# Kernel optimization log

Measured on AMD Instinct MI355X. Metric: run time of the kernel, lower is better.

The kernel has to match this reference:

```python
import jax, jax.numpy as jnp
import numpy as np

B, N, D_OBS, D_NB = 8192, 64, 128, 128
HEADS, GAT_F, GRU_H = 4, 64, 256
ACTION_DIM = 16
PERIOD0 = 24.0
NEG_SLOPE = 0.2
PMAX, PBUDGET = 0.5, 1.0
ENC_DIM = D_OBS + 1  # feature 0 expands to sin/cos
FUSE_IN = ENC_DIM + HEADS * GAT_F


def cyclical_encode(x):
    phase = 2.0 * jnp.pi * x[:, 0] / PERIOD0
    return jnp.concatenate([jnp.sin(phase)[:, None], jnp.cos(phase)[:, None], x[:, 1:]], axis=1)


def gat(node_feat, neigh_feat, mask, W, a):
    # node_feat [B,Din], neigh_feat [B,N,Din], W [Din,H*F], a [H,2F,1]
    b, n, _ = neigh_feat.shape
    h_node = (node_feat @ W).reshape(b, HEADS, GAT_F)            # [B,H,F]
    h_nb = (neigh_feat @ W).reshape(b, n, HEADS, GAT_F)          # [B,N,H,F]
    a_src, a_dst = a[:, :GAT_F, 0], a[:, GAT_F:, 0]              # [H,F] each
    e = (jnp.einsum('bhf,hf->bh', h_node, a_src)[:, None, :]
         + jnp.einsum('bnhf,hf->bnh', h_nb, a_dst))              # [B,N,H]
    e = jnp.where(e > 0, e, NEG_SLOPE * e)                        # leaky_relu
    e = jnp.where(mask[:, :, None], e, -jnp.inf)
    alpha = jax.nn.softmax(e, axis=1)                             # over neighbors
    agg = jnp.einsum('bnh,bnhf->bhf', alpha, h_nb)
    return agg.reshape(b, HEADS * GAT_F)


def gru_cell(x, h, Wih, bih, Whh, bhh):
    gi = x @ Wih + bih
    gh = h @ Whh + bhh
    ir, iz, in_ = jnp.split(gi, 3, axis=-1)
    hr, hz, hn = jnp.split(gh, 3, axis=-1)
    r = jax.nn.sigmoid(ir + hr)
    z = jax.nn.sigmoid(iz + hz)
    nn_ = jnp.tanh(in_ + r * hn)
    return (1.0 - z) * nn_ + z * h


def layer_norm(x, g, b, eps=1e-5):
    mu = jnp.mean(x, axis=-1, keepdims=True)
    var = jnp.var(x, axis=-1, keepdims=True)
    return (x - mu) * jax.lax.rsqrt(var + eps) * g + b


def project_power(raw):
    # Euclidean projection onto {0<=p<=PMAX, sum p<=PBUDGET} via bisection on mu
    def total(mu):
        return jnp.sum(jnp.clip(raw - mu[:, None], 0.0, PMAX), axis=1)
    feas = total(jnp.zeros(raw.shape[0], raw.dtype)) <= PBUDGET
    lo = jnp.zeros(raw.shape[0], raw.dtype)
    hi = jnp.maximum(jnp.max(raw, axis=1), 0.0)
    def body(_, lh):
        lo, hi = lh
        mid = 0.5 * (lo + hi)
        over = total(mid) > PBUDGET
        return (jnp.where(over, mid, lo), jnp.where(over, hi, mid))
    lo, hi = jax.lax.fori_loop(0, 60, body, (lo, hi))
    mu = jnp.where(feas, 0.0, hi)
    return jnp.clip(raw - mu[:, None], 0.0, PMAX)


def setup_inputs() -> dict:
    key = jax.random.key(0)
    ks = jax.random.split(key, 20)
    def init(k, shape, fan_in):
        return (jax.random.normal(k, shape, jnp.float32) / np.sqrt(fan_in)).astype(jnp.float32)
    mask = jax.random.bernoulli(ks[3], 0.5, (B, N))
    mask = mask.at[:, 0].set(True)  # guarantee >=1 valid neighbor per row
    return {
        'node_obs': jax.random.normal(ks[0], (B, D_OBS), jnp.float32),
        'neighbor_obs': jax.random.normal(ks[1], (B, N, D_NB), jnp.float32),
        'neighbor_mask': mask,
        'hidden_state': jnp.zeros((1, B, GRU_H), jnp.float32),
        'W_gat': init(ks[4], (D_NB, HEADS * GAT_F), D_NB),
        'a_gat': init(ks[5], (HEADS, 2 * GAT_F, 1), 2 * GAT_F),
        'fusion_W': init(ks[6], (FUSE_IN, GRU_H), FUSE_IN),
        'fusion_b': jnp.zeros((GRU_H,), jnp.float32),
        'Wih': init(ks[7], (GRU_H, 3 * GRU_H), GRU_H),
        'bih': jnp.zeros((3 * GRU_H,), jnp.float32),
        'Whh': init(ks[8], (GRU_H, 3 * GRU_H), GRU_H),
        'bhh': jnp.zeros((3 * GRU_H,), jnp.float32),
        'ln_g': jnp.ones((GRU_H,), jnp.float32),
        'ln_b': jnp.zeros((GRU_H,), jnp.float32),
        'W1': init(ks[9], (GRU_H, 256), GRU_H),
        'b1': jnp.zeros((256,), jnp.float32),
        'W2': init(ks[10], (256, 128), 256),
        'b2': jnp.zeros((128,), jnp.float32),
        'W3': init(ks[11], (128, ACTION_DIM), 128),
        'b3': jnp.zeros((ACTION_DIM,), jnp.float32),
    }


def reference(node_obs, neighbor_obs, neighbor_mask, hidden_state,
              W_gat, a_gat, fusion_W, fusion_b, Wih, bih, Whh, bhh,
              ln_g, ln_b, W1, b1, W2, b2, W3, b3):
    enc = cyclical_encode(node_obs)                              # [B, ENC_DIM]
    node_feat_for_gat = neighbor_obs[:, 0, :]
    ctx = gat(node_feat_for_gat, neighbor_obs, neighbor_mask, W_gat, a_gat)
    fused = jax.nn.relu(jnp.concatenate([enc, ctx], axis=-1) @ fusion_W + fusion_b)
    h_new = gru_cell(fused, hidden_state[0], Wih, bih, Whh, bhh)  # 1-step GRU
    belief = layer_norm(h_new, ln_g, ln_b)
    x = jax.nn.relu(belief @ W1 + b1)
    x = jax.nn.relu(x @ W2 + b2)
    raw = x @ W3 + b3                                            # [B, ACTION_DIM]
    action = project_power(raw)
    return action, h_new[None, :, :]
```

## Files before the change

### kernel.cpp

```cpp
#include <hip/hip_runtime.h>
#include <hip/hip_bf16.h>


typedef unsigned short u16;
typedef unsigned int   u32;
typedef __attribute__((ext_vector_type(8))) short bf16x8;
typedef __attribute__((ext_vector_type(4))) float f32x4;

#define KFUSE  672
#define ACT_TOT (8192*16)

__device__ __forceinline__ u16 f2bf(float x){
  u32 u = __float_as_uint(x);
  u += 0x7fffu + ((u >> 16) & 1u);
  return (u16)(u >> 16);
}
__device__ __forceinline__ float bf2f(u16 h){ return __uint_as_float(((u32)h) << 16); }

__device__ __forceinline__ void frag_one(const float* __restrict__ src, int ld, int col0,
                                         int NT, u16* __restrict__ dhi, u16* __restrict__ dlo,
                                         int f, int fsrc, int l){
  int kt = fsrc / NT, nt = fsrc % NT;
  int kbase = kt*32 + (l >> 4)*8, n = col0 + nt*16 + (l & 15);
  size_t o = ((size_t)f*64 + l)*8;
  #pragma unroll
  for(int i = 0; i < 8; ++i){
    float w = src[(size_t)(kbase + i)*ld + n];
    u16 h = f2bf(w);
    dhi[o + i] = h;
    dlo[o + i] = f2bf(w - bf2f(h));
  }
}

__device__ __forceinline__ void frag_wbig(const float* __restrict__ fW,
                                          const float* __restrict__ Wg,
                                          u16* __restrict__ dhi, u16* __restrict__ dlo,
                                          int f, int l){
  int kt = f / 16, nt = f % 16;
  int kbase = kt*32 + (l >> 4)*8, n = nt*16 + (l & 15);
  size_t o = ((size_t)f*64 + l)*8;
  #pragma unroll
  for(int i = 0; i < 8; ++i){
    int r = kbase + i;
    float v;
    if(r < 129) v = fW[(size_t)r*256 + n];
    else if(r < 641){
      int h = (r - 129) >> 7, kk = (r - 129) & 127;
      float s = 0.f;
      for(int ff = 0; ff < 64; ++ff)
        s += Wg[kk*256 + h*64 + ff] * fW[(size_t)(129 + h*64 + ff)*256 + n];
      v = s;
    } else v = 0.f;
    u16 hh = f2bf(v);
    dhi[o + i] = hh;
    dlo[o + i] = f2bf(v - bf2f(hh));
  }
}

#define P_FF0   1
#define P_WRZ0  85
#define P_WIN0  213
#define P_WHN0  245
#define P_F10   277
#define P_F20   309
#define P_SP0   325
__global__ __launch_bounds__(256) void k_prep(
    const unsigned char* __restrict__ maskb, int* __restrict__ flag,
    const float* __restrict__ Wg, const float* __restrict__ ag,
    float* __restrict__ was, float* __restrict__ wad,
    const float* __restrict__ fW,
    const float* __restrict__ Wih, const float* __restrict__ Whh,
    const float* __restrict__ W1, const float* __restrict__ W2,
    u16* __restrict__ ffh, u16* __restrict__ ffl,
    u16* __restrict__ wrzh, u16* __restrict__ wrzl,
    u16* __restrict__ winh, u16* __restrict__ winl,
    u16* __restrict__ whnh, u16* __restrict__ whnl,
    u16* __restrict__ f1h, u16* __restrict__ f1l,
    u16* __restrict__ f2h, u16* __restrict__ f2l,
    const float* __restrict__ hidden, u16* __restrict__ acath, u16* __restrict__ acatl)
{
  int bx = blockIdx.x, t = threadIdx.x;
  if(bx == 0){
    if(t == 0){
      int s = 0;
      for(int i = 1; i < 256; i += 4) s += maskb[i];
      *flag = (s == 0) ? 1 : 0;
    }
    #pragma unroll
    for(int v = 0; v < 2; ++v){
      int idx = v*256 + t, k = idx & 127, h = idx >> 7;
      float s = 0.f, d = 0.f;
      for(int f = 0; f < 64; ++f){
        float w = Wg[k*256 + h*64 + f];
        s += w * ag[h*128 + f];
        d += w * ag[h*128 + 64 + f];
      }
      was[k*4 + h] = s; wad[k*4 + h] = d;
    }
  } else if(bx < P_WRZ0){
    int sub = t >> 6, l = t & 63;
    int f = (bx - P_FF0)*4 + sub;
    frag_wbig(fW, Wg, ffh, ffl, f, l);
  } else if(bx < P_SP0){
    int sub = t >> 6, l = t & 63;
    if(bx < P_WIN0){
      int idx = (bx - P_WRZ0)*4 + sub;
      if(idx < 256) frag_one(Wih, 768, 0, 32, wrzh, wrzl, idx, idx, l);
      else          frag_one(Whh, 768, 0, 32, wrzh, wrzl, idx, idx - 256, l);
    } else if(bx < P_WHN0){
      int f = (bx - P_WIN0)*4 + sub;
      frag_one(Wih, 768, 512, 16, winh, winl, f, f, l);
    } else if(bx < P_F10){
      int f = (bx - P_WHN0)*4 + sub;
      frag_one(Whh, 768, 512, 16, whnh, whnl, f, f, l);
    } else if(bx < P_F20){
      int f = (bx - P_F10)*4 + sub;
      frag_one(W1, 256, 0, 16, f1h, f1l, f, f, l);
    } else {
      int f = (bx - P_F20)*4 + sub;
      frag_one(W2, 128, 0, 8, f2h, f2l, f, f, l);
    }
  } else {
    int i = (bx - P_SP0)*256 + t;
    int idx8 = i*8, row = idx8 >> 8, col = idx8 & 255;
    const float4* p = (const float4*)(hidden + (size_t)idx8);
    float4 v0 = p[0], v1 = p[1];
    float vv[8] = {v0.x,v0.y,v0.z,v0.w,v1.x,v1.y,v1.z,v1.w};
    u16 h8[8], l8[8];
    #pragma unroll
    for(int q = 0; q < 8; ++q){ u16 h = f2bf(vv[q]); h8[q] = h; l8[q] = f2bf(vv[q] - bf2f(h)); }
    uint4 uh = { (u32)h8[0] | ((u32)h8[1]<<16), (u32)h8[2] | ((u32)h8[3]<<16),
                 (u32)h8[4] | ((u32)h8[5]<<16), (u32)h8[6] | ((u32)h8[7]<<16) };
    uint4 ul = { (u32)l8[0] | ((u32)l8[1]<<16), (u32)l8[2] | ((u32)l8[3]<<16),
                 (u32)l8[4] | ((u32)l8[5]<<16), (u32)l8[6] | ((u32)l8[7]<<16) };
    size_t off = (size_t)row*512 + 256 + col;
    *(uint4*)(acath + off) = uh;
    *(uint4*)(acatl + off) = ul;
  }
}

__global__ __launch_bounds__(256) void k_gat(
    const float* __restrict__ nbg, const float* __restrict__ node,
    const void* __restrict__ maskp, const int* __restrict__ flagp,
    const float* __restrict__ was, const float* __restrict__ wad,
    u16* __restrict__ xhi, u16* __restrict__ xlo)
{
  __shared__ float s_nb[8192];
  __shared__ float s_wad[512];
  __shared__ float s_ep[1024];
  __shared__ float s_alpha[256];
  int b = blockIdx.x, t = threadIdx.x;
  const float* nb = nbg + (size_t)b*8192;
  const int isint = *flagp;

  s_wad[t] = wad[t]; s_wad[t+256] = wad[t+256];

  #pragma unroll
  for(int q = 0; q < 8; ++q){
    int f = q*256 + t;
    int n = f >> 5, ch = f & 31;
    float4 v = *(const float4*)(nb + f*4);
    *(float4*)(s_nb + (n*32 + (ch ^ (n & 31)))*4) = v;
  }

  if(t < 129){
    float v;
    if(t < 2){
      float ph = node[(size_t)b*128] * (6.2831853071795864769f / 24.0f);
      v = (t == 0) ? sinf(ph) : cosf(ph);
    } else v = node[(size_t)b*128 + (t-1)];
    u16 h = f2bf(v);
    size_t o = (size_t)b*KFUSE + t;
    xhi[o] = h; xlo[o] = f2bf(v - bf2f(h));
  } else if(t < 160){
    size_t o = (size_t)b*KFUSE + 641 + (t - 129);
    xhi[o] = 0; xlo[o] = 0;
  }
  __syncthreads();

  {
    int n = t & 63, c = t >> 6;
    float adx = 0.f, ady = 0.f, adz = 0.f, adw = 0.f;
    #pragma unroll
    for(int q = 0; q < 8; ++q){
      int ch = c*8 + q;
      float4 v = *(const float4*)(s_nb + (n*32 + (ch ^ (n & 31)))*4);
      float vv[4] = {v.x, v.y, v.z, v.w};
      #pragma unroll
      for(int i2 = 0; i2 < 4; ++i2){
        int k = ch*4 + i2;
        float4 wd = *(const float4*)(s_wad + k*4);
        adx += vv[i2]*wd.x; ady += vv[i2]*wd.y; adz += vv[i2]*wd.z; adw += vv[i2]*wd.w;
      }
    }
    float4 ad = {adx, ady, adz, adw};
    *(float4*)(s_ep + (c*64 + n)*4) = ad;
  }
  __syncthreads();

  {
    int n2 = t & 63, h2 = t >> 6;
    float es = 0.f;
    #pragma unroll
    for(int ii = 0; ii < 2; ++ii){
      int k = n2*2 + ii;
      float v0 = s_nb[(k >> 2)*4 + (k & 3)];
      es += v0 * was[k*4 + h2];
    }
    for(int off = 32; off; off >>= 1) es += __shfl_xor(es, off);
    float ed = s_ep[n2*4 + h2] + s_ep[(64+n2)*4 + h2]
             + s_ep[(128+n2)*4 + h2] + s_ep[(192+n2)*4 + h2];
    float e = es + ed;
    e = (e > 0.f) ? e : 0.2f*e;
    bool valid;
    if(isint) valid = ((const u32*)maskp)[(size_t)b*64 + n2] != 0u;
    else      valid = ((const unsigned char*)maskp)[(size_t)b*64 + n2] != 0;
    float ev = valid ? e : -1e30f;
    float m = ev;
    for(int off = 32; off; off >>= 1) m = fmaxf(m, __shfl_xor(m, off));
    float p = valid ? expf(ev - m) : 0.f;
    float s = p;
    for(int off = 32; off; off >>= 1) s += __shfl_xor(s, off);
    s_alpha[n2*4 + h2] = p / s;
  }
  __syncthreads();

  {
    int c2 = t & 31, hp = (t >> 6) & 1, half = t >> 7;
    int sub = (t >> 5) & 1;
    float4 a0 = {0.f,0.f,0.f,0.f}, a1 = {0.f,0.f,0.f,0.f};
    int nbase = half*32 + sub*16;
    #pragma unroll
    for(int i = 0; i < 16; ++i){
      int n = nbase + i;
      float4 v = *(const float4*)(s_nb + (n*32 + (c2 ^ (n & 31)))*4);
      float2 ap = *(const float2*)(s_alpha + n*4 + hp*2);
      a0.x += ap.x*v.x; a0.y += ap.x*v.y; a0.z += ap.x*v.z; a0.w += ap.x*v.w;
      a1.x += ap.y*v.x; a1.y += ap.y*v.y; a1.z += ap.y*v.z; a1.w += ap.y*v.w;
    }
    a0.x += __shfl_xor(a0.x, 32); a0.y += __shfl_xor(a0.y, 32);
    a0.z += __shfl_xor(a0.z, 32); a0.w += __shfl_xor(a0.w, 32);
    a1.x += __shfl_xor(a1.x, 32); a1.y += __shfl_xor(a1.y, 32);
    a1.z += __shfl_xor(a1.z, 32); a1.w += __shfl_xor(a1.w, 32);
    __syncthreads();
    if((t & 63) < 32){
      int w = t >> 6;
      *(float4*)(s_ep + (w*32 + c2)*8 + 0) = a0;
      *(float4*)(s_ep + (w*32 + c2)*8 + 4) = a1;
    }
  }
  __syncthreads();
  if(t < 128){
    int h = t >> 5, cc = t & 31;
    int hp2 = h >> 1, slot = h & 1;
    float4 p0 = *(const float4*)(s_ep + ((0*2 + hp2)*32 + cc)*8 + slot*4);
    float4 p1 = *(const float4*)(s_ep + ((1*2 + hp2)*32 + cc)*8 + slot*4);
    float vv[4] = {p0.x+p1.x, p0.y+p1.y, p0.z+p1.z, p0.w+p1.w};
    size_t o = (size_t)b*KFUSE + 129 + h*128 + cc*4;
    #pragma unroll
    for(int i = 0; i < 4; ++i){
      u16 hh = f2bf(vv[i]);
      xhi[o+i] = hh; xlo[o+i] = f2bf(vv[i] - bf2f(hh));
    }
  }
}

template<int KT, int NT_TOT, int NPW, int ROWF>
__global__ __launch_bounds__(256) void k_gemm3(
    const u16* __restrict__ xhi, const u16* __restrict__ xlo, int lda,
    const u16* __restrict__ wfhi, const u16* __restrict__ wflo,
    const float* __restrict__ bias,
    u16* __restrict__ ohi, u16* __restrict__ olo, int ost, int ocol)
{
  int l = threadIdx.x & 63, w = threadIdx.x >> 6;
  int m0 = blockIdx.x * (16*ROWF);
  int ntbase = blockIdx.y * (4*NPW) + w*NPW;
  f32x4 acc[NPW][ROWF];
  #pragma unroll
  for(int j = 0; j < NPW; ++j)
    #pragma unroll
    for(int rf = 0; rf < ROWF; ++rf) acc[j][rf] = (f32x4){0.f,0.f,0.f,0.f};
  size_t arow[ROWF];
  #pragma unroll
  for(int rf = 0; rf < ROWF; ++rf)
    arow[rf] = (size_t)(m0 + rf*16 + (l & 15))*lda + (size_t)((l >> 4)*8);
  bf16x8 ah[ROWF], al[ROWF];
  #pragma unroll
  for(int rf = 0; rf < ROWF; ++rf){
    ah[rf] = *(const bf16x8*)(xhi + arow[rf]);
    al[rf] = *(const bf16x8*)(xlo + arow[rf]);
  }
  for(int kt = 0; kt < KT; ++kt){
    bf16x8 ahn[ROWF], aln[ROWF];
    if(kt + 1 < KT){
      #pragma unroll
      for(int rf = 0; rf < ROWF; ++rf){
        ahn[rf] = *(const bf16x8*)(xhi + arow[rf] + (kt+1)*32);
        aln[rf] = *(const bf16x8*)(xlo + arow[rf] + (kt+1)*32);
      }
    }
    #pragma unroll
    for(int j = 0; j < NPW; ++j){
      size_t bo = ((size_t)(kt*NT_TOT + ntbase + j)*64 + l)*8;
      bf16x8 bh = *(const bf16x8*)(wfhi + bo);
      bf16x8 bl = *(const bf16x8*)(wflo + bo);
      #pragma unroll
      for(int rf = 0; rf < ROWF; ++rf){
        acc[j][rf] = __builtin_amdgcn_mfma_f32_16x16x32_bf16(ah[rf], bh, acc[j][rf], 0, 0, 0);
        acc[j][rf] = __builtin_amdgcn_mfma_f32_16x16x32_bf16(ah[rf], bl, acc[j][rf], 0, 0, 0);
        acc[j][rf] = __builtin_amdgcn_mfma_f32_16x16x32_bf16(al[rf], bh, acc[j][rf], 0, 0, 0);
      }
    }
    #pragma unroll
    for(int rf = 0; rf < ROWF; ++rf){ ah[rf] = ahn[rf]; al[rf] = aln[rf]; }
  }
  #pragma unroll
  for(int j = 0; j < NPW; ++j){
    int col = (ntbase + j)*16 + (l & 15);
    float bv = bias[col];
    #pragma unroll
    for(int rf = 0; rf < ROWF; ++rf){
      int r0 = m0 + rf*16 + (l >> 4)*4;
      #pragma unroll
      for(int q = 0; q < 4; ++q){
        float y = fmaxf(acc[j][rf][q] + bv, 0.f);
        size_t o = (size_t)(r0 + q)*ost + ocol + col;
        u16 h = f2bf(y);
        ohi[o] = h; olo[o] = f2bf(y - bf2f(h));
      }
    }
  }
}

#define BSTR 264
#define XSTR 132
__global__ __launch_bounds__(512) void k_grumlp(
    const u16* __restrict__ ah_, const u16* __restrict__ al_,
    const u16* __restrict__ wrzh, const u16* __restrict__ wrzl,
    const u16* __restrict__ winh, const u16* __restrict__ winl,
    const u16* __restrict__ whnh, const u16* __restrict__ whnl,
    const u16* __restrict__ f1h, const u16* __restrict__ f1l,
    const u16* __restrict__ f2h, const u16* __restrict__ f2l,
    const float* __restrict__ bih, const float* __restrict__ bhh,
    const float* __restrict__ hidden, const float* __restrict__ lng,
    const float* __restrict__ lnb,
    const float* __restrict__ b1, const float* __restrict__ b2,
    const float* __restrict__ W3, const float* __restrict__ b3,
    float* __restrict__ hout, float* __restrict__ act)
{
  __shared__ float s_s1[256], s_s2[256], s_mu[32], s_rs[32];
  __shared__ u16 s_bh[32*BSTR], s_bl[32*BSTR];
  __shared__ float s_x2[32*XSTR];
  __shared__ float sW3[2048];
  int t = threadIdx.x;
  int l = t & 63, w = t >> 6;
  int m0 = blockIdx.x*32;
  for(int i = t; i < 2048; i += 512) sW3[i] = W3[i];

  f32x4 ar[2][2], az[2][2], aa[2][2], ab[2][2];
  #pragma unroll
  for(int j = 0; j < 2; ++j)
    #pragma unroll
    for(int rf = 0; rf < 2; ++rf){
      ar[j][rf] = (f32x4){0.f,0.f,0.f,0.f}; az[j][rf] = (f32x4){0.f,0.f,0.f,0.f};
      aa[j][rf] = (f32x4){0.f,0.f,0.f,0.f}; ab[j][rf] = (f32x4){0.f,0.f,0.f,0.f};
    }
  size_t arow[2];
  #pragma unroll
  for(int rf = 0; rf < 2; ++rf)
    arow[rf] = (size_t)(m0 + rf*16 + (l & 15))*512 + (size_t)((l >> 4)*8);
  for(int kt = 0; kt < 16; ++kt){
    bf16x8 xh[2], xl[2];
    #pragma unroll
    for(int rf = 0; rf < 2; ++rf){
      xh[rf] = *(const bf16x8*)(ah_ + arow[rf] + kt*32);
      xl[rf] = *(const bf16x8*)(al_ + arow[rf] + kt*32);
    }
    #pragma unroll
    for(int j = 0; j < 2; ++j){
      int nt = w*2 + j;
      size_t bo = ((size_t)(kt*32 + nt)*64 + l)*8;
      bf16x8 bh = *(const bf16x8*)(wrzh + bo);
      bf16x8 bl = *(const bf16x8*)(wrzl + bo);
      size_t bo2 = bo + (size_t)16*64*8;
      bf16x8 bh2 = *(const bf16x8*)(wrzh + bo2);
      bf16x8 bl2 = *(const bf16x8*)(wrzl + bo2);
      #pragma unroll
      for(int rf = 0; rf < 2; ++rf){
        ar[j][rf] = __builtin_amdgcn_mfma_f32_16x16x32_bf16(xh[rf], bh, ar[j][rf], 0, 0, 0);
        ar[j][rf] = __builtin_amdgcn_mfma_f32_16x16x32_bf16(xh[rf], bl, ar[j][rf], 0, 0, 0);
        ar[j][rf] = __builtin_amdgcn_mfma_f32_16x16x32_bf16(xl[rf], bh, ar[j][rf], 0, 0, 0);
        az[j][rf] = __builtin_amdgcn_mfma_f32_16x16x32_bf16(xh[rf], bh2, az[j][rf], 0, 0, 0);
        az[j][rf] = __builtin_amdgcn_mfma_f32_16x16x32_bf16(xh[rf], bl2, az[j][rf], 0, 0, 0);
        az[j][rf] = __builtin_amdgcn_mfma_f32_16x16x32_bf16(xl[rf], bh2, az[j][rf], 0, 0, 0);
      }
    }
  }
  for(int kt = 0; kt < 8; ++kt){
    bf16x8 fh[2], fl2[2], gh[2], gl[2];
    #pragma unroll
    for(int rf = 0; rf < 2; ++rf){
      fh[rf]  = *(const bf16x8*)(ah_ + arow[rf] + kt*32);
      fl2[rf] = *(const bf16x8*)(al_ + arow[rf] + kt*32);
      gh[rf]  = *(const bf16x8*)(ah_ + arow[rf] + 256 + kt*32);
      gl[rf]  = *(const bf16x8*)(al_ + arow[rf] + 256 + kt*32);
    }
    #pragma unroll
    for(int j = 0; j < 2; ++j){
      int nt = w*2 + j;
      size_t bo = ((size_t)(kt*16 + nt)*64 + l)*8;
      bf16x8 bh = *(const bf16x8*)(winh + bo);
      bf16x8 bl = *(const bf16x8*)(winl + bo);
      bf16x8 ch = *(const bf16x8*)(whnh + bo);
      bf16x8 cl2 = *(const bf16x8*)(whnl + bo);
      #pragma unroll
      for(int rf = 0; rf < 2; ++rf){
        aa[j][rf] = __builtin_amdgcn_mfma_f32_16x16x32_bf16(fh[rf], bh, aa[j][rf], 0, 0, 0);
        aa[j][rf] = __builtin_amdgcn_mfma_f32_16x16x32_bf16(fh[rf], bl, aa[j][rf], 0, 0, 0);
        aa[j][rf] = __builtin_amdgcn_mfma_f32_16x16x32_bf16(fl2[rf], bh, aa[j][rf], 0, 0, 0);
        ab[j][rf] = __builtin_amdgcn_mfma_f32_16x16x32_bf16(gh[rf], ch, ab[j][rf], 0, 0, 0);
        ab[j][rf] = __builtin_amdgcn_mfma_f32_16x16x32_bf16(gh[rf], cl2, ab[j][rf], 0, 0, 0);
        ab[j][rf] = __builtin_amdgcn_mfma_f32_16x16x32_bf16(gl[rf], ch, ab[j][rf], 0, 0, 0);
      }
    }
  }
  int cl = l & 15, rq = l >> 4;
  float hnew[2][2][4];
  float s1p[2][4], s2p[2][4];
  #pragma unroll
  for(int rf = 0; rf < 2; ++rf)
    #pragma unroll
    for(int q = 0; q < 4; ++q){ s1p[rf][q] = 0.f; s2p[rf][q] = 0.f; }
  #pragma unroll
  for(int j = 0; j < 2; ++j){
    int col = w*32 + j*16 + cl;
    float br = bih[col] + bhh[col];
    float bz = bih[256+col] + bhh[256+col];
    float bi = bih[512+col];
    float bh2 = bhh[512+col];
    #pragma unroll
    for(int rf = 0; rf < 2; ++rf){
      #pragma unroll
      for(int q = 0; q < 4; ++q){
        int row = m0 + rf*16 + rq*4 + q;
        float rs = ar[j][rf][q] + br;
        float zs = az[j][rf][q] + bz;
        float in_ = aa[j][rf][q] + bi;
        float hn  = ab[j][rf][q] + bh2;
        float h   = hidden[(size_t)row*256 + col];
        float r = 1.f/(1.f + expf(-rs));
        float z = 1.f/(1.f + expf(-zs));
        float nv = tanhf(in_ + r*hn);
        float hv = (1.f - z)*nv + z*h;
        hnew[j][rf][q] = hv;
        hout[(size_t)row*256 + col] = hv;
        s1p[rf][q] += hv; s2p[rf][q] += hv*hv;
      }
    }
  }
  #pragma unroll
  for(int rf = 0; rf < 2; ++rf)
    #pragma unroll
    for(int q = 0; q < 4; ++q){
      float a = s1p[rf][q], b2v = s2p[rf][q];
      for(int off = 1; off < 16; off <<= 1){
        a += __shfl_xor(a, off); b2v += __shfl_xor(b2v, off);
      }
      if(cl == 0){
        int rloc = rf*16 + rq*4 + q;
        s_s1[w*32 + rloc] = a; s_s2[w*32 + rloc] = b2v;
      }
    }
  __syncthreads();
  if(t < 32){
    int rloc = t;
    float t1 = 0.f, t2 = 0.f;
    #pragma unroll
    for(int ww = 0; ww < 8; ++ww){ t1 += s_s1[ww*32 + rloc]; t2 += s_s2[ww*32 + rloc]; }
    float mu = t1 * (1.f/256.f);
    float var = t2 * (1.f/256.f) - mu*mu;
    s_mu[rloc] = mu; s_rs[rloc] = rsqrtf(var + 1e-5f);
  }
  __syncthreads();
  #pragma unroll
  for(int j = 0; j < 2; ++j){
    int col = w*32 + j*16 + cl;
    float g = lng[col], bb = lnb[col];
    #pragma unroll
    for(int rf = 0; rf < 2; ++rf){
      #pragma unroll
      for(int q = 0; q < 4; ++q){
        int rloc = rf*16 + rq*4 + q;
        float bel = (hnew[j][rf][q] - s_mu[rloc]) * s_rs[rloc] * g + bb;
        u16 hb = f2bf(bel);
        s_bh[rloc*BSTR + col] = hb;
        s_bl[rloc*BSTR + col] = f2bf(bel - bf2f(hb));
      }
    }
  }
  __syncthreads();
  f32x4 ax1[2][2];
  #pragma unroll
  for(int j = 0; j < 2; ++j)
    #pragma unroll
    for(int rf = 0; rf < 2; ++rf) ax1[j][rf] = (f32x4){0.f,0.f,0.f,0.f};
  for(int kt = 0; kt < 8; ++kt){
    bf16x8 xh[2], xl[2];
    #pragma unroll
    for(int rf = 0; rf < 2; ++rf){
      int off = (rf*16 + (l & 15))*BSTR + kt*32 + (l >> 4)*8;
      xh[rf] = *(const bf16x8*)(s_bh + off);
      xl[rf] = *(const bf16x8*)(s_bl + off);
    }
    #pragma unroll
    for(int j = 0; j < 2; ++j){
      size_t bo = ((size_t)(kt*16 + w*2 + j)*64 + l)*8;
      bf16x8 bh = *(const bf16x8*)(f1h + bo);
      bf16x8 bl = *(const bf16x8*)(f1l + bo);
      #pragma unroll
      for(int rf = 0; rf < 2; ++rf){
        ax1[j][rf] = __builtin_amdgcn_mfma_f32_16x16x32_bf16(xh[rf], bh, ax1[j][rf], 0, 0, 0);
        ax1[j][rf] = __builtin_amdgcn_mfma_f32_16x16x32_bf16(xh[rf], bl, ax1[j][rf], 0, 0, 0);
        ax1[j][rf] = __builtin_amdgcn_mfma_f32_16x16x32_bf16(xl[rf], bh, ax1[j][rf], 0, 0, 0);
      }
    }
  }
  __syncthreads();
  #pragma unroll
  for(int j = 0; j < 2; ++j){
    int col = (w*2 + j)*16 + cl;
    float bv = b1[col];
    #pragma unroll
    for(int rf = 0; rf < 2; ++rf){
      #pragma unroll
      for(int q = 0; q < 4; ++q){
        int rloc = rf*16 + rq*4 + q;
        float y = fmaxf(ax1[j][rf][q] + bv, 0.f);
        u16 hh = f2bf(y);
        s_bh[rloc*BSTR + col] = hh;
        s_bl[rloc*BSTR + col] = f2bf(y - bf2f(hh));
      }
    }
  }
  __syncthreads();
  f32x4 ax2[2];
  #pragma unroll
  for(int rf = 0; rf < 2; ++rf) ax2[rf] = (f32x4){0.f,0.f,0.f,0.f};
  for(int kt = 0; kt < 8; ++kt){
    bf16x8 xh[2], xl[2];
    #pragma unroll
    for(int rf = 0; rf < 2; ++rf){
      int off = (rf*16 + (l & 15))*BSTR + kt*32 + (l >> 4)*8;
      xh[rf] = *(const bf16x8*)(s_bh + off);
      xl[rf] = *(const bf16x8*)(s_bl + off);
    }
    size_t bo = ((size_t)(kt*8 + w)*64 + l)*8;
    bf16x8 bh = *(const bf16x8*)(f2h + bo);
    bf16x8 bl = *(const bf16x8*)(f2l + bo);
    #pragma unroll
    for(int rf = 0; rf < 2; ++rf){
      ax2[rf] = __builtin_amdgcn_mfma_f32_16x16x32_bf16(xh[rf], bh, ax2[rf], 0, 0, 0);
      ax2[rf] = __builtin_amdgcn_mfma_f32_16x16x32_bf16(xh[rf], bl, ax2[rf], 0, 0, 0);
      ax2[rf] = __builtin_amdgcn_mfma_f32_16x16x32_bf16(xl[rf], bh, ax2[rf], 0, 0, 0);
    }
  }
  {
    int col = w*16 + cl;
    float bv = b2[col];
    #pragma unroll
    for(int rf = 0; rf < 2; ++rf)
      #pragma unroll
      for(int q = 0; q < 4; ++q){
        int rloc = rf*16 + rq*4 + q;
        s_x2[rloc*XSTR + col] = fmaxf(ax2[rf][q] + bv, 0.f);
      }
  }
  __syncthreads();
  {
    int j = t & 15, rl = t >> 4;
    const float* xr = s_x2 + rl*XSTR;
    float raw = b3[j];
    #pragma unroll 8
    for(int k4 = 0; k4 < 32; ++k4){
      float4 v = *(const float4*)(xr + k4*4);
      raw += v.x*sW3[(k4*4+0)*16 + j] + v.y*sW3[(k4*4+1)*16 + j]
           + v.z*sW3[(k4*4+2)*16 + j] + v.w*sW3[(k4*4+3)*16 + j];
    }
    float c0 = fminf(fmaxf(raw, 0.f), 0.5f);
    float tot = c0;
    for(int off = 8; off; off >>= 1) tot += __shfl_xor(tot, off);
    float mx = raw;
    for(int off = 8; off; off >>= 1) mx = fmaxf(mx, __shfl_xor(mx, off));
    bool feas = (tot <= 1.0f);
    float lo = 0.f, hi = fmaxf(mx, 0.f);
    for(int it = 0; it < 60; ++it){
      float mid = 0.5f*(lo + hi);
      float s = fminf(fmaxf(raw - mid, 0.f), 0.5f);
      for(int off = 8; off; off >>= 1) s += __shfl_xor(s, off);
      bool over = s > 1.0f;
      lo = over ? mid : lo;
      hi = over ? hi : mid;
    }
    float muv = feas ? 0.f : hi;
    act[(size_t)(m0 + rl)*16 + j] = fminf(fmaxf(raw - muv, 0.f), 0.5f);
  }
}

#define OFF_FLAG   0u
#define OFF_WAS    4096u
#define OFF_WAD    8192u
#define OFF_FFH    12288u
#define OFF_FFL    356352u
#define OFF_WRZH   700416u
#define OFF_WRZL   1224704u
#define OFF_WINH   1748992u
#define OFF_WINL   1880064u
#define OFF_WHNH   2011136u
#define OFF_WHNL   2142208u
#define OFF_F1H    2273280u
#define OFF_F1L    2404352u
#define OFF_F2H    2535424u
#define OFF_F2L    2600960u
#define OFF_XCATH  2666496u
#define OFF_XCATL  13676544u
#define OFF_ACATH  24686592u
#define OFF_ACATL  33075200u

extern "C" void kernel_launch(void* const* d_in, const int* in_sizes, int n_in,
                              void* d_out, int out_size, void* d_ws, size_t ws_size,
                              hipStream_t stream){
  const float* node   = (const float*)d_in[0];
  const float* nbr    = (const float*)d_in[1];
  const void*  mask   = d_in[2];
  const float* hidden = (const float*)d_in[3];
  const float* Wg     = (const float*)d_in[4];
  const float* ag     = (const float*)d_in[5];
  const float* fW     = (const float*)d_in[6];
  const float* fb     = (const float*)d_in[7];
  const float* Wih    = (const float*)d_in[8];
  const float* bih    = (const float*)d_in[9];
  const float* Whh    = (const float*)d_in[10];
  const float* bhh    = (const float*)d_in[11];
  const float* lng    = (const float*)d_in[12];
  const float* lnb    = (const float*)d_in[13];
  const float* W1     = (const float*)d_in[14];
  const float* b1     = (const float*)d_in[15];
  const float* W2     = (const float*)d_in[16];
  const float* b2     = (const float*)d_in[17];
  const float* W3     = (const float*)d_in[18];
  const float* b3     = (const float*)d_in[19];
  char* ws = (char*)d_ws;
  float* out = (float*)d_out;

  int*   flag = (int*)  (ws + OFF_FLAG);
  float* was  = (float*)(ws + OFF_WAS);
  float* wad  = (float*)(ws + OFF_WAD);
  u16* ffh  = (u16*)(ws + OFF_FFH);   u16* ffl  = (u16*)(ws + OFF_FFL);
  u16* wrzh = (u16*)(ws + OFF_WRZH);  u16* wrzl = (u16*)(ws + OFF_WRZL);
  u16* winh = (u16*)(ws + OFF_WINH);  u16* winl = (u16*)(ws + OFF_WINL);
  u16* whnh = (u16*)(ws + OFF_WHNH);  u16* whnl = (u16*)(ws + OFF_WHNL);
  u16* f1h  = (u16*)(ws + OFF_F1H);   u16* f1l  = (u16*)(ws + OFF_F1L);
  u16* f2h  = (u16*)(ws + OFF_F2H);   u16* f2l  = (u16*)(ws + OFF_F2L);
  u16* xh   = (u16*)(ws + OFF_XCATH); u16* xl   = (u16*)(ws + OFF_XCATL);
  u16* ach  = (u16*)(ws + OFF_ACATH); u16* acl  = (u16*)(ws + OFF_ACATL);

  k_prep<<<1349, 256, 0, stream>>>((const unsigned char*)mask, flag, Wg, ag, was, wad,
                                   fW, Wih, Whh, W1, W2,
                                   ffh, ffl, wrzh, wrzl, winh, winl, whnh, whnl,
                                   f1h, f1l, f2h, f2l, hidden, ach, acl);

  k_gat<<<8192, 256, 0, stream>>>(nbr, node, mask, flag, was, wad, xh, xl);

  k_gemm3<21,16,2,4><<<dim3(128,2), 256, 0, stream>>>(xh, xl, KFUSE, ffh, ffl, fb, ach, acl, 512, 0);

  k_grumlp<<<256, 512, 0, stream>>>(ach, acl, wrzh, wrzl, winh, winl, whnh, whnl,
                                    f1h, f1l, f2h, f2l, bih, bhh, hidden, lng, lnb,
                                    b1, b2, W3, b3, out + ACT_TOT, out);
}
```

Measured before the change: 179.0 us.

## Move hidden-state split into GAT kernel, prefetch GEMM B fragments, drop LDS wad

Moves the hidden-state bf16 hi/lo split from the prep kernel into extra blocks appended to the GAT launch, which shortens the serial prep kernel. The GAT kernel now reads wad from global memory at a wave-uniform address instead of staging it in shared memory, which removes an LDS fill. The fusion GEMM also double-buffers its weight fragments, loading the next k-step's B fragments alongside the A prefetch. In exchange, GEMM register pressure rises and GAT blocks take on more global/scalar loads.

```diff
diff --git a/kernel.cpp b/kernel.cpp
--- a/kernel.cpp
+++ b/kernel.cpp
@@ -63,7 +63,6 @@
 #define P_WHN0  245
 #define P_F10   277
 #define P_F20   309
-#define P_SP0   325
 __global__ __launch_bounds__(256) void k_prep(
     const unsigned char* __restrict__ maskb, int* __restrict__ flag,
     const float* __restrict__ Wg, const float* __restrict__ ag,
@@ -76,8 +75,7 @@
     u16* __restrict__ winh, u16* __restrict__ winl,
     u16* __restrict__ whnh, u16* __restrict__ whnl,
     u16* __restrict__ f1h, u16* __restrict__ f1l,
-    u16* __restrict__ f2h, u16* __restrict__ f2l,
-    const float* __restrict__ hidden, u16* __restrict__ acath, u16* __restrict__ acatl)
+    u16* __restrict__ f2h, u16* __restrict__ f2l)
 {
   int bx = blockIdx.x, t = threadIdx.x;
   if(bx == 0){
@@ -101,7 +99,7 @@
     int sub = t >> 6, l = t & 63;
     int f = (bx - P_FF0)*4 + sub;
     frag_wbig(fW, Wg, ffh, ffl, f, l);
-  } else if(bx < P_SP0){
+  } else {
     int sub = t >> 6, l = t & 63;
     if(bx < P_WIN0){
       int idx = (bx - P_WRZ0)*4 + sub;
@@ -120,8 +118,20 @@
       int f = (bx - P_F20)*4 + sub;
       frag_one(W2, 128, 0, 8, f2h, f2l, f, f, l);
     }
-  } else {
-    int i = (bx - P_SP0)*256 + t;
+  }
+}
+
+__global__ __launch_bounds__(256) void k_gat(
+    const float* __restrict__ nbg, const float* __restrict__ node,
+    const void* __restrict__ maskp, const int* __restrict__ flagp,
+    const float* __restrict__ was, const float* __restrict__ wad,
+    u16* __restrict__ xhi, u16* __restrict__ xlo,
+    const float* __restrict__ hidden,
+    u16* __restrict__ acath, u16* __restrict__ acatl)
+{
+  int t = threadIdx.x;
+  if(blockIdx.x >= 8192){
+    int i = (blockIdx.x - 8192)*256 + t;
     int idx8 = i*8, row = idx8 >> 8, col = idx8 & 255;
     const float4* p = (const float4*)(hidden + (size_t)idx8);
     float4 v0 = p[0], v1 = p[1];
@@ -136,24 +146,15 @@
     size_t off = (size_t)row*512 + 256 + col;
     *(uint4*)(acath + off) = uh;
     *(uint4*)(acatl + off) = ul;
-  }
-}
-
-__global__ __launch_bounds__(256) void k_gat(
-    const float* __restrict__ nbg, const float* __restrict__ node,
-    const void* __restrict__ maskp, const int* __restrict__ flagp,
-    const float* __restrict__ was, const float* __restrict__ wad,
-    u16* __restrict__ xhi, u16* __restrict__ xlo)
-{
+    return;
+  }
+
   __shared__ float s_nb[8192];
-  __shared__ float s_wad[512];
   __shared__ float s_ep[1024];
   __shared__ float s_alpha[256];
-  int b = blockIdx.x, t = threadIdx.x;
+  int b = blockIdx.x;
   const float* nb = nbg + (size_t)b*8192;
   const int isint = *flagp;
-
-  s_wad[t] = wad[t]; s_wad[t+256] = wad[t+256];
 
   #pragma unroll
   for(int q = 0; q < 8; ++q){
@@ -180,6 +181,8 @@
 
   {
     int n = t & 63, c = t >> 6;
+    int cu = __builtin_amdgcn_readfirstlane(c);
+    const float* wadc = wad + cu*128;
     float adx = 0.f, ady = 0.f, adz = 0.f, adw = 0.f;
     #pragma unroll
     for(int q = 0; q < 8; ++q){
@@ -188,8 +191,7 @@
       float vv[4] = {v.x, v.y, v.z, v.w};
       #pragma unroll
       for(int i2 = 0; i2 < 4; ++i2){
-        int k = ch*4 + i2;
-        float4 wd = *(const float4*)(s_wad + k*4);
+        float4 wd = *(const float4*)(wadc + (q*4 + i2)*4);
         adx += vv[i2]*wd.x; ady += vv[i2]*wd.y; adz += vv[i2]*wd.z; adw += vv[i2]*wd.w;
       }
     }
@@ -284,35 +286,46 @@
   #pragma unroll
   for(int rf = 0; rf < ROWF; ++rf)
     arow[rf] = (size_t)(m0 + rf*16 + (l & 15))*lda + (size_t)((l >> 4)*8);
-  bf16x8 ah[ROWF], al[ROWF];
+  bf16x8 ah[ROWF], al[ROWF], bhc[NPW], blc[NPW];
   #pragma unroll
   for(int rf = 0; rf < ROWF; ++rf){
     ah[rf] = *(const bf16x8*)(xhi + arow[rf]);
     al[rf] = *(const bf16x8*)(xlo + arow[rf]);
   }
+  #pragma unroll
+  for(int j = 0; j < NPW; ++j){
+    size_t bo = ((size_t)(ntbase + j)*64 + l)*8;
+    bhc[j] = *(const bf16x8*)(wfhi + bo);
+    blc[j] = *(const bf16x8*)(wflo + bo);
+  }
   for(int kt = 0; kt < KT; ++kt){
-    bf16x8 ahn[ROWF], aln[ROWF];
+    bf16x8 ahn[ROWF], aln[ROWF], bhn[NPW], bln[NPW];
     if(kt + 1 < KT){
       #pragma unroll
       for(int rf = 0; rf < ROWF; ++rf){
         ahn[rf] = *(const bf16x8*)(xhi + arow[rf] + (kt+1)*32);
         aln[rf] = *(const bf16x8*)(xlo + arow[rf] + (kt+1)*32);
       }
+      #pragma unroll
+      for(int j = 0; j < NPW; ++j){
+        size_t bo = ((size_t)((kt+1)*NT_TOT + ntbase + j)*64 + l)*8;
+        bhn[j] = *(const bf16x8*)(wfhi + bo);
+        bln[j] = *(const bf16x8*)(wflo + bo);
+      }
     }
     #pragma unroll
     for(int j = 0; j < NPW; ++j){
-      size_t bo = ((size_t)(kt*NT_TOT + ntbase + j)*64 + l)*8;
-      bf16x8 bh = *(const bf16x8*)(wfhi + bo);
-      bf16x8 bl = *(const bf16x8*)(wflo + bo);
       #pragma unroll
       for(int rf = 0; rf < ROWF; ++rf){
-        acc[j][rf] = __builtin_amdgcn_mfma_f32_16x16x32_bf16(ah[rf], bh, acc[j][rf], 0, 0, 0);
-        acc[j][rf] = __builtin_amdgcn_mfma_f32_16x16x32_bf16(ah[rf], bl, acc[j][rf], 0, 0, 0);
-        acc[j][rf] = __builtin_amdgcn_mfma_f32_16x16x32_bf16(al[rf], bh, acc[j][rf], 0, 0, 0);
+        acc[j][rf] = __builtin_amdgcn_mfma_f32_16x16x32_bf16(ah[rf], bhc[j], acc[j][rf], 0, 0, 0);
+        acc[j][rf] = __builtin_amdgcn_mfma_f32_16x16x32_bf16(ah[rf], blc[j], acc[j][rf], 0, 0, 0);
+        acc[j][rf] = __builtin_amdgcn_mfma_f32_16x16x32_bf16(al[rf], bhc[j], acc[j][rf], 0, 0, 0);
       }
     }
     #pragma unroll
     for(int rf = 0; rf < ROWF; ++rf){ ah[rf] = ahn[rf]; al[rf] = aln[rf]; }
+    #pragma unroll
+    for(int j = 0; j < NPW; ++j){ bhc[j] = bhn[j]; blc[j] = bln[j]; }
   }
   #pragma unroll
   for(int j = 0; j < NPW; ++j){
@@ -664,12 +677,13 @@
   u16* xh   = (u16*)(ws + OFF_XCATH); u16* xl   = (u16*)(ws + OFF_XCATL);
   u16* ach  = (u16*)(ws + OFF_ACATH); u16* acl  = (u16*)(ws + OFF_ACATL);
 
-  k_prep<<<1349, 256, 0, stream>>>((const unsigned char*)mask, flag, Wg, ag, was, wad,
-                                   fW, Wih, Whh, W1, W2,
-                                   ffh, ffl, wrzh, wrzl, winh, winl, whnh, whnl,
-                                   f1h, f1l, f2h, f2l, hidden, ach, acl);
-
-  k_gat<<<8192, 256, 0, stream>>>(nbr, node, mask, flag, was, wad, xh, xl);
+  k_prep<<<325, 256, 0, stream>>>((const unsigned char*)mask, flag, Wg, ag, was, wad,
+                                  fW, Wih, Whh, W1, W2,
+                                  ffh, ffl, wrzh, wrzl, winh, winl, whnh, whnl,
+                                  f1h, f1l, f2h, f2l);
+
+  k_gat<<<8192 + 1024, 256, 0, stream>>>(nbr, node, mask, flag, was, wad, xh, xl,
+                                         hidden, ach, acl);
 
   k_gemm3<21,16,2,4><<<dim3(128,2), 256, 0, stream>>>(xh, xl, KFUSE, ffh, ffl, fb, ach, acl, 512, 0);
 
```

New measurement: 178.6 us. Within noise of the previous version (-0.2%).
